# Kernel tuning notes

Measured on AMD Instinct MI355X. Metric: run time of the kernel, lower is better.

The kernel has to match this reference:

```python
import jax, jax.numpy as jnp
import numpy as np

B, S, H, F, E, K = 4, 2048, 1024, 3584, 8, 2
CAP_FACTOR = 1.25


def setup_inputs() -> dict:
    key = jax.random.key(0)
    k1, k2, k3, k4, k5 = jax.random.split(key, 5)
    s_h = 1.0 / np.sqrt(H)
    s_f = 1.0 / np.sqrt(F)
    return {
        "hidden_states": jax.random.normal(k1, (B, S, H), dtype=jnp.float32),
        "gate_w": jax.random.normal(k2, (E, H), dtype=jnp.float32) * s_h,
        "w1": jax.random.normal(k3, (E, H, F), dtype=jnp.float32) * s_h,
        "w2": jax.random.normal(k4, (E, F, H), dtype=jnp.float32) * s_f,
        "w3": jax.random.normal(k5, (E, H, F), dtype=jnp.float32) * s_h,
    }


def _moe_forward(hidden_states, gate_w, w1, w2, w3):
    b, s, h = hidden_states.shape
    dtype = hidden_states.dtype
    x = hidden_states.reshape(-1, h)  # [B*S, H]
    router_logits = x @ gate_w.T  # [B*S, E]
    expert_weights = jax.nn.softmax(router_logits.astype(jnp.float32), axis=1)
    _, selected_experts = jax.lax.top_k(expert_weights, K)  # [B*S, K]

    top_k_idx = selected_experts.reshape(b, s, K)
    probs = expert_weights.reshape(b, s, E)

    capacity = int(s * K / E * CAP_FACTOR)  # expert capacity per batch

    # dispatch/combine masks (Mixtral 'dropping' implementation)
    expert_mask = jax.nn.one_hot(top_k_idx, E, dtype=jnp.int32)  # [b,s,K,E]
    mask_fused = expert_mask.reshape(b, s * K, E)
    count_fused = jnp.cumsum(mask_fused, axis=1)  # running count per expert
    count = count_fused.reshape(b, s, K, E)
    trunc_mask = expert_mask * (count <= capacity).astype(jnp.int32)
    combined_mask = trunc_mask.sum(axis=2)  # [b,s,E]
    masked_probs = probs * combined_mask  # drop over-capacity tokens

    pos_fused = mask_fused * count_fused
    pos = pos_fused.reshape(b, s, K, E)
    combined_pos = pos.sum(axis=2) * combined_mask  # [b,s,E], 1-based slot
    pos_in_cap = jax.nn.one_hot(combined_pos, capacity + 1, dtype=jnp.int32)
    combine_mask = masked_probs[..., None] * pos_in_cap  # [b,s,E,cap+1]
    combine_mask = combine_mask[..., 1:].astype(dtype)  # drop slot 0 (dropped tokens)
    dispatch_mask = (combine_mask != 0).astype(dtype)  # [b,s,E,cap]

    # dispatch tokens into per-expert capacity buffers
    dispatch = jnp.einsum('bsm,bsec->ebcm', hidden_states, dispatch_mask)
    # expert FFN (SwiGLU)
    h1 = jnp.einsum('ebcm,emh->ebch', dispatch, w1)
    h3 = jnp.einsum('ebcm,emh->ebch', dispatch, w3)
    expert_out = jnp.einsum('ebch,ehm->ebcm', jax.nn.silu(h1) * h3, w2)
    # combine back to token order with routing probabilities
    final = jnp.einsum('ebcm,bsec->bsm', expert_out, combine_mask)
    return final


def reference(hidden_states, gate_w, w1, w2, w3):
    return _moe_forward(hidden_states, gate_w, w1, w2, w3)
```

## Files before the change

kernel.cpp:

```cpp
#include <hip/hip_runtime.h>
#include <hip/hip_bf16.h>
#include <math.h>

#define B_   4
#define S_   2048
#define H_   1024
#define F_   3584
#define E_   8
#define TOPK 2
#define CAP  640
#define M_   (B_*CAP)
#define NTOK (B_*S_)

typedef __attribute__((ext_vector_type(8))) short short8;
typedef __attribute__((ext_vector_type(4))) float f32x4;
typedef __attribute__((ext_vector_type(4))) unsigned short us4;

static __device__ __forceinline__ unsigned short f2bf(float f) {
  __hip_bfloat16 h = __float2bfloat16(f);
  return *reinterpret_cast<unsigned short*>(&h);
}
static __device__ __forceinline__ float bf2f(unsigned short u) {
  unsigned int x = ((unsigned int)u) << 16;
  float f;
  __builtin_memcpy(&f, &x, 4);
  return f;
}

static __device__ __forceinline__ void gload16(const void* g, void* l) {
  __builtin_amdgcn_global_load_lds((const __attribute__((address_space(1))) void*)g,
                                   (__attribute__((address_space(3))) void*)l, 16, 0, 0);
}

#define BAR() __builtin_amdgcn_s_barrier()
#define WLG() asm volatile("s_waitcnt lgkmcnt(0)" ::: "memory")
#define VM2() asm volatile("s_waitcnt vmcnt(2)" ::: "memory")
#define VM0() asm volatile("s_waitcnt vmcnt(0)" ::: "memory")

__global__ __launch_bounds__(64) void k_router(const float* __restrict__ hs,
                                               const float* __restrict__ gw,
                                               int* __restrict__ e01,
                                               float* __restrict__ p01,
                                               unsigned short* __restrict__ hsb) {
  int t = blockIdx.x;
  int lane = threadIdx.x;
  const float4* xv = (const float4*)(hs + (size_t)t * H_);
  float4 xr[4];
#pragma unroll
  for (int i = 0; i < 4; ++i) xr[i] = xv[lane + i * 64];
#pragma unroll
  for (int i = 0; i < 4; ++i) {
    us4 v = {f2bf(xr[i].x), f2bf(xr[i].y), f2bf(xr[i].z), f2bf(xr[i].w)};
    *(us4*)&hsb[(size_t)t * H_ + (size_t)(lane + i * 64) * 4] = v;
  }
  float logit[E_];
#pragma unroll
  for (int e = 0; e < E_; ++e) {
    const float4* gv = (const float4*)(gw + (size_t)e * H_);
    float acc = 0.f;
#pragma unroll
    for (int i = 0; i < 4; ++i) {
      float4 g = gv[lane + i * 64];
      acc += xr[i].x * g.x + xr[i].y * g.y + xr[i].z * g.z + xr[i].w * g.w;
    }
#pragma unroll
    for (int off = 32; off > 0; off >>= 1) acc += __shfl_xor(acc, off);
    logit[e] = acc;
  }
  float mx = logit[0];
#pragma unroll
  for (int e = 1; e < E_; ++e) mx = fmaxf(mx, logit[e]);
  float p[E_], s = 0.f;
#pragma unroll
  for (int e = 0; e < E_; ++e) { p[e] = expf(logit[e] - mx); s += p[e]; }
  float inv = 1.f / s;
  int e0 = 0;
#pragma unroll
  for (int e = 1; e < E_; ++e) if (p[e] > p[e0]) e0 = e;
  int e1 = (e0 == 0) ? 1 : 0;
#pragma unroll
  for (int e = 0; e < E_; ++e) if (e != e0 && p[e] > p[e1]) e1 = e;
  if (lane == 0) {
    e01[t * 2 + 0] = e0;
    e01[t * 2 + 1] = e1;
    p01[t * 2 + 0] = p[e0] * inv;
    p01[t * 2 + 1] = p[e1] * inv;
  }
}

__global__ __launch_bounds__(256) void k_positions(const int* __restrict__ e01,
                                                   int* __restrict__ pos,
                                                   int* __restrict__ disp) {
  int b = blockIdx.x, tid = threadIdx.x;
  __shared__ unsigned char eid[S_ * TOPK];
  __shared__ int part[256];
  for (int i = tid; i < E_ * CAP; i += 256)
    disp[((size_t)(i / CAP) * B_ + b) * CAP + (i % CAP)] = -1;
  for (int i = tid; i < S_ * TOPK; i += 256)
    eid[i] = (unsigned char)e01[b * S_ * TOPK + i];
  __syncthreads();
  const int per = (S_ * TOPK) / 256;
  int base = tid * per;
  for (int e = 0; e < E_; ++e) {
    int cnt = 0;
    for (int j = 0; j < per; ++j) cnt += (eid[base + j] == e) ? 1 : 0;
    part[tid] = cnt;
    __syncthreads();
    for (int off = 1; off < 256; off <<= 1) {
      int v = part[tid];
      int add = (tid >= off) ? part[tid - off] : 0;
      __syncthreads();
      part[tid] = v + add;
      __syncthreads();
    }
    int run = part[tid] - cnt;
    for (int j = 0; j < per; ++j) {
      int sl = base + j;
      if (eid[sl] == e) {
        ++run;
        int p = (run <= CAP) ? (run - 1) : -1;
        pos[b * S_ * TOPK + sl] = p;
        if (p >= 0) disp[((size_t)e * B_ + b) * CAP + p] = sl >> 1;
      }
    }
    __syncthreads();
  }
}

__global__ __launch_bounds__(256) void k_transpose(const float* __restrict__ in,
                                                   unsigned short* __restrict__ outp,
                                                   int R, int C, int ileave, int half,
                                                   size_t ostride_e) {
  __shared__ unsigned short ls[64][72];
  int e = blockIdx.z, tc = blockIdx.x, tr = blockIdx.y, tid = threadIdx.x;
  const float* src = in + (size_t)e * R * C + (size_t)tr * 64 * C + (size_t)tc * 64;
#pragma unroll
  for (int i = 0; i < 16; ++i) {
    int row = i * 4 + (tid >> 6), col = tid & 63;
    ls[row][col] = f2bf(src[(size_t)row * C + col]);
  }
  __syncthreads();
  unsigned short* dbase = outp + (size_t)e * ostride_e;
#pragma unroll
  for (int i = 0; i < 4; ++i) {
    int orow = i * 16 + (tid >> 4), oc = (tid & 15) * 4;
    int gr = tc * 64 + orow;
    int ri = ileave ? ((gr & ~15) * 2 + (gr & 15) + half * 16) : gr;
    us4 v = {ls[oc + 0][orow], ls[oc + 1][orow], ls[oc + 2][orow], ls[oc + 3][orow]};
    *(us4*)&dbase[(size_t)ri * R + tr * 64 + oc] = v;
  }
}

#define STAGE_A(d, h, t) {                                                    \
    gload16(pA0 + (size_t)(t) * 64 + (h) * 32, &lds[((d) * 2 + (h)) * 8192 + tid * 8]); \
  }
#define STAGE_B(d, h, t) {                                                    \
    gload16(srcB + (size_t)(t) * 64 + (h) * 32, &lds[32768 + ((d) * 2 + (h)) * 8192 + tid * 8]); \
  }
#define RD_A4(d, h) {                                                         \
    const unsigned short* _pa = &lds[((d) * 2 + (h)) * 8192 + aoff];          \
    _Pragma("unroll") for (int m = 0; m < 4; ++m)                             \
      a[m] = *(const short8*)&_pa[m * 512];                                   \
  }
#define RD_B4(d, h) {                                                         \
    const unsigned short* _pb = &lds[32768 + ((d) * 2 + (h)) * 8192 + boff];  \
    _Pragma("unroll") for (int n = 0; n < 4; ++n)                             \
      b[n] = *(const short8*)&_pb[n * 512];                                   \
  }
#define MFMA16() {                                                            \
    __builtin_amdgcn_s_setprio(1);                                            \
    _Pragma("unroll") for (int m = 0; m < 4; ++m)                             \
      _Pragma("unroll") for (int n = 0; n < 4; ++n)                           \
        acc[m][n] = __builtin_amdgcn_mfma_f32_16x16x32_bf16(a[m], b[n], acc[m][n], 0, 0, 0); \
    __builtin_amdgcn_s_setprio(0);                                            \
  }
#define BODY(P, tn) {                                                         \
    RD_A4(P, 0); RD_B4(P, 0); STAGE_A((P) ^ 1, 0, tn); STAGE_B((P) ^ 1, 0, tn); \
    WLG(); MFMA16(); VM2(); BAR();                                            \
    RD_A4(P, 1); RD_B4(P, 1); STAGE_A((P) ^ 1, 1, tn); STAGE_B((P) ^ 1, 1, tn); \
    WLG(); MFMA16(); VM2(); BAR();                                            \
  }
#define PEEL(P) {                                                             \
    RD_A4(P, 0); RD_B4(P, 0);                                                 \
    WLG(); MFMA16(); VM0(); BAR();                                            \
    RD_A4(P, 1); RD_B4(P, 1);                                                 \
    WLG(); MFMA16();                                                          \
  }

template <int KTOT, bool SWIGLU, bool GATHER, int MT, int NTN, int NTOTB, int SPLITK>
__global__ __launch_bounds__(1024, 4) void k_gemm256(const unsigned short* __restrict__ Aall,
                                                     const unsigned short* __restrict__ Ball,
                                                     unsigned short* __restrict__ Cout,
                                                     const int* __restrict__ disp) {
  constexpr int KSUB = KTOT / SPLITK;
  constexpr int NT = KSUB / 64;
  __shared__ __align__(16) unsigned short lds[65536];

  const int nwg = MT * NTN * E_ * SPLITK;
  int lid = blockIdx.x;
  int sw = (lid & 7) * (nwg >> 3) + (lid >> 3);
  constexpr int PER = MT * NTN;
  int ks = sw / (PER * E_);
  int rem2 = sw - ks * (PER * E_);
  int e = rem2 / PER;
  int rem = rem2 - e * PER;
  int tn = rem / MT, tm = rem - tn * MT;

  int tid = threadIdx.x, li = tid & 63, wid = tid >> 6;
  int wm = wid >> 2, wn = wid & 3;

  int rS = tid >> 2;
  int gS = (tid & 3) ^ ((tid >> 3) & 3);
  const unsigned short* pA0;
  if constexpr (GATHER) {
    int r0 = tm * 256 + rS;
    int b0 = r0 / CAP;
    int tok0 = disp[(size_t)e * B_ * CAP + r0];
    if (tok0 < 0) tok0 = 0;
    pA0 = Aall + ((size_t)b0 * S_ + tok0) * H_ + ks * KSUB + gS * 8;
  } else {
    pA0 = Aall + ((size_t)e * M_ + (size_t)tm * 256 + rS) * KTOT + ks * KSUB + gS * 8;
  }
  const unsigned short* srcB = Ball + ((size_t)e * NTOTB + (size_t)tn * 256 + rS) * KTOT + ks * KSUB + gS * 8;

  int sA = (li >> 4) ^ ((li >> 1) & 3);
  int aoff = (wm * 64 + (li & 15)) * 32 + sA * 8;
  int boff = (wn * 64 + (li & 15)) * 32 + sA * 8;

  f32x4 acc[4][4] = {};
  short8 a[4], b[4];

  STAGE_A(0, 0, 0); STAGE_B(0, 0, 0);
  STAGE_A(0, 1, 0); STAGE_B(0, 1, 0);
  VM2();
  BAR();

#pragma unroll 1
  for (int t = 0; t + 1 < NT - 1; t += 2) {
    BODY(0, t + 1);
    BODY(1, t + 2);
  }
  if constexpr (((NT - 1) & 1) != 0) {
    BODY(0, NT - 1);
  }
  if constexpr (((NT - 1) & 1) != 0) {
    PEEL(1);
  } else {
    PEEL(0);
  }

  int r0o = tm * 256 + wm * 64 + ((li >> 4) << 2);
  if constexpr (SWIGLU) {
    unsigned short* out = Cout + (size_t)e * M_ * F_;
#pragma unroll
    for (int m = 0; m < 4; ++m)
#pragma unroll
      for (int u = 0; u < 2; ++u) {
        int col = (tn * 8 + wn * 2 + u) * 16 + (li & 15);
#pragma unroll
        for (int j = 0; j < 4; ++j) {
          float h1 = acc[m][2 * u][j], h3 = acc[m][2 * u + 1][j];
          float sg = 1.f / (1.f + __expf(-h1));
          out[(size_t)(r0o + m * 16 + j) * F_ + col] = f2bf(h1 * sg * h3);
        }
      }
  } else {
    unsigned short* out = Cout + ((size_t)ks * E_ + e) * M_ * NTOTB;
#pragma unroll
    for (int m = 0; m < 4; ++m)
#pragma unroll
      for (int n = 0; n < 4; ++n) {
        int col = tn * 256 + wn * 64 + n * 16 + (li & 15);
#pragma unroll
        for (int j = 0; j < 4; ++j)
          out[(size_t)(r0o + m * 16 + j) * NTOTB + col] = f2bf(acc[m][n][j]);
      }
  }
}

__global__ __launch_bounds__(256) void k_combine(const unsigned short* __restrict__ Oe0,
                                                 const unsigned short* __restrict__ Oe1,
                                                 const int* __restrict__ e01,
                                                 const float* __restrict__ p01,
                                                 const int* __restrict__ pos,
                                                 float* __restrict__ outp) {
  int t = blockIdx.x;
  int b = t / S_;
  int tid = threadIdx.x;
  float4 acc = {0.f, 0.f, 0.f, 0.f};
#pragma unroll
  for (int k = 0; k < TOPK; ++k) {
    int p = pos[t * 2 + k];
    if (p >= 0) {
      int e = e01[t * 2 + k];
      float w = p01[t * 2 + k];
      size_t row = (size_t)e * M_ + (size_t)b * CAP + p;
      us4 v0 = *(const us4*)&Oe0[row * H_ + tid * 4];
      us4 v1 = *(const us4*)&Oe1[row * H_ + tid * 4];
      acc.x += w * (bf2f(v0[0]) + bf2f(v1[0]));
      acc.y += w * (bf2f(v0[1]) + bf2f(v1[1]));
      acc.z += w * (bf2f(v0[2]) + bf2f(v1[2]));
      acc.w += w * (bf2f(v0[3]) + bf2f(v1[3]));
    }
  }
  *(float4*)&outp[(size_t)t * H_ + tid * 4] = acc;
}

extern "C" void kernel_launch(void* const* d_in, const int* in_sizes, int n_in,
                              void* d_out, int out_size, void* d_ws, size_t ws_size,
                              hipStream_t stream) {
  const float* hs = (const float*)d_in[0];
  const float* gw = (const float*)d_in[1];
  const float* w1 = (const float*)d_in[2];
  const float* w2 = (const float*)d_in[3];
  const float* w3 = (const float*)d_in[4];

  char* ws = (char*)d_ws;
  size_t off = 0;
  auto take = [&](size_t bytes) -> char* {
    char* p = ws + off;
    off += (bytes + 255) & ~(size_t)255;
    return p;
  };
  int*            e01  = (int*)take((size_t)NTOK * 2 * 4);
  float*          p01  = (float*)take((size_t)NTOK * 2 * 4);
  int*            pos  = (int*)take((size_t)NTOK * 2 * 4);
  int*            disp = (int*)take((size_t)E_ * B_ * CAP * 4);
  unsigned short* w13t = (unsigned short*)take((size_t)E_ * 2 * F_ * H_ * 2);
  unsigned short* w2t  = (unsigned short*)take((size_t)E_ * H_ * F_ * 2);
  unsigned short* hsb  = (unsigned short*)take((size_t)NTOK * H_ * 2);
  unsigned short* act  = (unsigned short*)take((size_t)E_ * M_ * F_ * 2);
  unsigned short* oe   = (unsigned short*)take((size_t)2 * E_ * M_ * H_ * 2);

  k_router<<<NTOK, 64, 0, stream>>>(hs, gw, e01, p01, hsb);
  k_positions<<<B_, 256, 0, stream>>>(e01, pos, disp);
  k_transpose<<<dim3(F_ / 64, H_ / 64, E_), 256, 0, stream>>>(w1, w13t, H_, F_, 1, 0, (size_t)2 * F_ * H_);
  k_transpose<<<dim3(F_ / 64, H_ / 64, E_), 256, 0, stream>>>(w3, w13t, H_, F_, 1, 1, (size_t)2 * F_ * H_);
  k_transpose<<<dim3(H_ / 64, F_ / 64, E_), 256, 0, stream>>>(w2, w2t, F_, H_, 0, 0, (size_t)H_ * F_);
  k_gemm256<H_, true, true, M_ / 256, (2 * F_) / 256, 2 * F_, 1>
      <<<(M_ / 256) * ((2 * F_) / 256) * E_, 1024, 0, stream>>>(hsb, w13t, act, disp);
  k_gemm256<F_, false, false, M_ / 256, H_ / 256, H_, 2>
      <<<(M_ / 256) * (H_ / 256) * E_ * 2, 1024, 0, stream>>>(act, w2t, oe, disp);
  k_combine<<<NTOK, 256, 0, stream>>>(oe, oe + (size_t)E_ * M_ * H_, e01, p01, pos, (float*)d_out);
}
```

Baseline: 599.2 us.

## Split GEMM kernels and give down-projection 512-thread blocks with 128x64 warp tiles

The shared templated GEMM becomes two kernels. The gate/up kernel keeps its 1024-thread, 64x64-per-warp layout. The down-projection kernel now runs 512 threads per block, and each warp covers a 128x64 output tile with 8x4 accumulators. Each thread issues two global-to-LDS loads per stage, and the pipeline is split into four MFMA phases with vmcnt(4) waits. The aim is more operand reuse per LDS read and per wave, at the cost of a doubled accumulator register footprint and lower occupancy.

New measurement: 614.0 us. +2.5%, slower.

```diff
diff --git a/kernel.cpp b/kernel.cpp
--- a/kernel.cpp
+++ b/kernel.cpp
@@ -34,6 +34,7 @@
 
 #define BAR() __builtin_amdgcn_s_barrier()
 #define WLG() asm volatile("s_waitcnt lgkmcnt(0)" ::: "memory")
+#define VM4() asm volatile("s_waitcnt vmcnt(4)" ::: "memory")
 #define VM2() asm volatile("s_waitcnt vmcnt(2)" ::: "memory")
 #define VM0() asm volatile("s_waitcnt vmcnt(0)" ::: "memory")
 
@@ -151,47 +152,164 @@
   }
 }
 
-#define STAGE_A(d, h, t) {                                                    \
+#define STAGE_A10(d, h, t) {                                                  \
     gload16(pA0 + (size_t)(t) * 64 + (h) * 32, &lds[((d) * 2 + (h)) * 8192 + tid * 8]); \
   }
-#define STAGE_B(d, h, t) {                                                    \
+#define STAGE_B10(d, h, t) {                                                  \
     gload16(srcB + (size_t)(t) * 64 + (h) * 32, &lds[32768 + ((d) * 2 + (h)) * 8192 + tid * 8]); \
   }
-#define RD_A4(d, h) {                                                         \
+#define RD_A10(d, h) {                                                        \
     const unsigned short* _pa = &lds[((d) * 2 + (h)) * 8192 + aoff];          \
     _Pragma("unroll") for (int m = 0; m < 4; ++m)                             \
       a[m] = *(const short8*)&_pa[m * 512];                                   \
   }
-#define RD_B4(d, h) {                                                         \
+#define RD_B10(d, h) {                                                        \
     const unsigned short* _pb = &lds[32768 + ((d) * 2 + (h)) * 8192 + boff];  \
     _Pragma("unroll") for (int n = 0; n < 4; ++n)                             \
       b[n] = *(const short8*)&_pb[n * 512];                                   \
   }
-#define MFMA16() {                                                            \
+#define MFMA10() {                                                            \
     __builtin_amdgcn_s_setprio(1);                                            \
     _Pragma("unroll") for (int m = 0; m < 4; ++m)                             \
       _Pragma("unroll") for (int n = 0; n < 4; ++n)                           \
         acc[m][n] = __builtin_amdgcn_mfma_f32_16x16x32_bf16(a[m], b[n], acc[m][n], 0, 0, 0); \
     __builtin_amdgcn_s_setprio(0);                                            \
   }
-#define BODY(P, tn) {                                                         \
-    RD_A4(P, 0); RD_B4(P, 0); STAGE_A((P) ^ 1, 0, tn); STAGE_B((P) ^ 1, 0, tn); \
-    WLG(); MFMA16(); VM2(); BAR();                                            \
-    RD_A4(P, 1); RD_B4(P, 1); STAGE_A((P) ^ 1, 1, tn); STAGE_B((P) ^ 1, 1, tn); \
-    WLG(); MFMA16(); VM2(); BAR();                                            \
-  }
-#define PEEL(P) {                                                             \
-    RD_A4(P, 0); RD_B4(P, 0);                                                 \
-    WLG(); MFMA16(); VM0(); BAR();                                            \
-    RD_A4(P, 1); RD_B4(P, 1);                                                 \
-    WLG(); MFMA16();                                                          \
-  }
-
-template <int KTOT, bool SWIGLU, bool GATHER, int MT, int NTN, int NTOTB, int SPLITK>
-__global__ __launch_bounds__(1024, 4) void k_gemm256(const unsigned short* __restrict__ Aall,
-                                                     const unsigned short* __restrict__ Ball,
-                                                     unsigned short* __restrict__ Cout,
-                                                     const int* __restrict__ disp) {
+#define BODY10(P, tn) {                                                       \
+    RD_A10(P, 0); RD_B10(P, 0); STAGE_A10((P) ^ 1, 0, tn); STAGE_B10((P) ^ 1, 0, tn); \
+    WLG(); MFMA10(); VM2(); BAR();                                            \
+    RD_A10(P, 1); RD_B10(P, 1); STAGE_A10((P) ^ 1, 1, tn); STAGE_B10((P) ^ 1, 1, tn); \
+    WLG(); MFMA10(); VM2(); BAR();                                            \
+  }
+#define PEEL10(P) {                                                           \
+    RD_A10(P, 0); RD_B10(P, 0);                                               \
+    WLG(); MFMA10(); VM0(); BAR();                                            \
+    RD_A10(P, 1); RD_B10(P, 1);                                               \
+    WLG(); MFMA10();                                                          \
+  }
+
+template <int KTOT, int MT, int NTN, int NTOTB>
+__global__ __launch_bounds__(1024, 4) void k_gemm1(const unsigned short* __restrict__ Aall,
+                                                   const unsigned short* __restrict__ Ball,
+                                                   unsigned short* __restrict__ Cout,
+                                                   const int* __restrict__ disp) {
+  constexpr int NT = KTOT / 64;
+  __shared__ __align__(16) unsigned short lds[65536];
+
+  const int nwg = MT * NTN * E_;
+  int lid = blockIdx.x;
+  int sw = (lid & 7) * (nwg >> 3) + (lid >> 3);
+  constexpr int PER = MT * NTN;
+  int e = sw / PER;
+  int rem = sw - e * PER;
+  int tn = rem / MT, tm = rem - tn * MT;
+
+  int tid = threadIdx.x, li = tid & 63, wid = tid >> 6;
+  int wm = wid >> 2, wn = wid & 3;
+
+  int rS = tid >> 2;
+  int gS = (tid & 3) ^ ((tid >> 3) & 3);
+  int r0 = tm * 256 + rS;
+  int b0 = r0 / CAP;
+  int tok0 = disp[(size_t)e * B_ * CAP + r0];
+  if (tok0 < 0) tok0 = 0;
+  const unsigned short* pA0 = Aall + ((size_t)b0 * S_ + tok0) * H_ + gS * 8;
+  const unsigned short* srcB = Ball + ((size_t)e * NTOTB + (size_t)tn * 256 + rS) * KTOT + gS * 8;
+
+  int sA = (li >> 4) ^ ((li >> 1) & 3);
+  int aoff = (wm * 64 + (li & 15)) * 32 + sA * 8;
+  int boff = (wn * 64 + (li & 15)) * 32 + sA * 8;
+
+  f32x4 acc[4][4] = {};
+  short8 a[4], b[4];
+
+  STAGE_A10(0, 0, 0); STAGE_B10(0, 0, 0);
+  STAGE_A10(0, 1, 0); STAGE_B10(0, 1, 0);
+  VM2();
+  BAR();
+
+#pragma unroll 1
+  for (int t = 0; t + 1 < NT - 1; t += 2) {
+    BODY10(0, t + 1);
+    BODY10(1, t + 2);
+  }
+  if constexpr (((NT - 1) & 1) != 0) {
+    BODY10(0, NT - 1);
+  }
+  if constexpr (((NT - 1) & 1) != 0) {
+    PEEL10(1);
+  } else {
+    PEEL10(0);
+  }
+
+  int r0o = tm * 256 + wm * 64 + ((li >> 4) << 2);
+  unsigned short* out = Cout + (size_t)e * M_ * F_;
+#pragma unroll
+  for (int m = 0; m < 4; ++m)
+#pragma unroll
+    for (int u = 0; u < 2; ++u) {
+      int col = (tn * 8 + wn * 2 + u) * 16 + (li & 15);
+#pragma unroll
+      for (int j = 0; j < 4; ++j) {
+        float h1 = acc[m][2 * u][j], h3 = acc[m][2 * u + 1][j];
+        float sg = 1.f / (1.f + __expf(-h1));
+        out[(size_t)(r0o + m * 16 + j) * F_ + col] = f2bf(h1 * sg * h3);
+      }
+    }
+}
+
+#define STAGE_A5(d, h, t) {                                                   \
+    size_t _o = (size_t)(t) * 64 + (h) * 32;                                  \
+    gload16(pA0 + _o, &lds[((d) * 2 + (h)) * 8192 + tid * 8]);                \
+    gload16(pA1 + _o, &lds[((d) * 2 + (h)) * 8192 + tid * 8 + 4096]);         \
+  }
+#define STAGE_B5(d, h, t) {                                                   \
+    size_t _o = (size_t)(t) * 64 + (h) * 32;                                  \
+    gload16(srcB + _o, &lds[32768 + ((d) * 2 + (h)) * 8192 + tid * 8]);       \
+    gload16(srcB + (size_t)128 * KTOT + _o, &lds[32768 + ((d) * 2 + (h)) * 8192 + tid * 8 + 4096]); \
+  }
+#define RD_A5(d, h, mh) {                                                     \
+    const unsigned short* _pa = &lds[((d) * 2 + (h)) * 8192 + aoff + (mh) * 2048]; \
+    _Pragma("unroll") for (int j = 0; j < 4; ++j)                             \
+      a[j] = *(const short8*)&_pa[j * 512];                                   \
+  }
+#define RD_B5(d, h) {                                                         \
+    const unsigned short* _pb = &lds[32768 + ((d) * 2 + (h)) * 8192 + boff];  \
+    _Pragma("unroll") for (int n = 0; n < 4; ++n)                             \
+      b[n] = *(const short8*)&_pb[n * 512];                                   \
+  }
+#define MFMA5(mh) {                                                           \
+    __builtin_amdgcn_s_setprio(1);                                            \
+    _Pragma("unroll") for (int j = 0; j < 4; ++j)                             \
+      _Pragma("unroll") for (int n = 0; n < 4; ++n)                           \
+        acc[(mh) * 4 + j][n] = __builtin_amdgcn_mfma_f32_16x16x32_bf16(a[j], b[n], acc[(mh) * 4 + j][n], 0, 0, 0); \
+    __builtin_amdgcn_s_setprio(0);                                            \
+  }
+#define BODY5(P, tn) {                                                        \
+    RD_A5(P, 0, 0); RD_B5(P, 0); STAGE_A5((P) ^ 1, 0, tn);                    \
+    WLG(); MFMA5(0); BAR();                                                   \
+    RD_A5(P, 0, 1); STAGE_B5((P) ^ 1, 0, tn);                                 \
+    WLG(); MFMA5(1); VM4(); BAR();                                            \
+    RD_A5(P, 1, 0); RD_B5(P, 1); STAGE_A5((P) ^ 1, 1, tn);                    \
+    WLG(); MFMA5(0); BAR();                                                   \
+    RD_A5(P, 1, 1); STAGE_B5((P) ^ 1, 1, tn);                                 \
+    WLG(); MFMA5(1); VM4(); BAR();                                            \
+  }
+#define PEEL5(P) {                                                            \
+    RD_A5(P, 0, 0); RD_B5(P, 0);                                              \
+    WLG(); MFMA5(0); BAR();                                                   \
+    RD_A5(P, 0, 1);                                                           \
+    WLG(); MFMA5(1); VM0(); BAR();                                            \
+    RD_A5(P, 1, 0); RD_B5(P, 1);                                              \
+    WLG(); MFMA5(0); BAR();                                                   \
+    RD_A5(P, 1, 1);                                                           \
+    WLG(); MFMA5(1);                                                          \
+  }
+
+template <int KTOT, int MT, int NTN, int NTOTB, int SPLITK>
+__global__ __launch_bounds__(512, 2) void k_gemm2(const unsigned short* __restrict__ Aall,
+                                                  const unsigned short* __restrict__ Ball,
+                                                  unsigned short* __restrict__ Cout) {
   constexpr int KSUB = KTOT / SPLITK;
   constexpr int NT = KSUB / 64;
   __shared__ __align__(16) unsigned short lds[65536];
@@ -211,71 +329,47 @@
 
   int rS = tid >> 2;
   int gS = (tid & 3) ^ ((tid >> 3) & 3);
-  const unsigned short* pA0;
-  if constexpr (GATHER) {
-    int r0 = tm * 256 + rS;
-    int b0 = r0 / CAP;
-    int tok0 = disp[(size_t)e * B_ * CAP + r0];
-    if (tok0 < 0) tok0 = 0;
-    pA0 = Aall + ((size_t)b0 * S_ + tok0) * H_ + ks * KSUB + gS * 8;
-  } else {
-    pA0 = Aall + ((size_t)e * M_ + (size_t)tm * 256 + rS) * KTOT + ks * KSUB + gS * 8;
-  }
+  const unsigned short* pA0 = Aall + ((size_t)e * M_ + (size_t)tm * 256 + rS) * KTOT + ks * KSUB + gS * 8;
+  const unsigned short* pA1 = pA0 + (size_t)128 * KTOT;
   const unsigned short* srcB = Ball + ((size_t)e * NTOTB + (size_t)tn * 256 + rS) * KTOT + ks * KSUB + gS * 8;
 
   int sA = (li >> 4) ^ ((li >> 1) & 3);
-  int aoff = (wm * 64 + (li & 15)) * 32 + sA * 8;
+  int aoff = (wm * 128 + (li & 15)) * 32 + sA * 8;
   int boff = (wn * 64 + (li & 15)) * 32 + sA * 8;
 
-  f32x4 acc[4][4] = {};
+  f32x4 acc[8][4] = {};
   short8 a[4], b[4];
 
-  STAGE_A(0, 0, 0); STAGE_B(0, 0, 0);
-  STAGE_A(0, 1, 0); STAGE_B(0, 1, 0);
-  VM2();
+  STAGE_A5(0, 0, 0); STAGE_B5(0, 0, 0);
+  STAGE_A5(0, 1, 0); STAGE_B5(0, 1, 0);
+  VM4();
   BAR();
 
 #pragma unroll 1
   for (int t = 0; t + 1 < NT - 1; t += 2) {
-    BODY(0, t + 1);
-    BODY(1, t + 2);
+    BODY5(0, t + 1);
+    BODY5(1, t + 2);
   }
   if constexpr (((NT - 1) & 1) != 0) {
-    BODY(0, NT - 1);
+    BODY5(0, NT - 1);
   }
   if constexpr (((NT - 1) & 1) != 0) {
-    PEEL(1);
+    PEEL5(1);
   } else {
-    PEEL(0);
-  }
-
-  int r0o = tm * 256 + wm * 64 + ((li >> 4) << 2);
-  if constexpr (SWIGLU) {
-    unsigned short* out = Cout + (size_t)e * M_ * F_;
-#pragma unroll
-    for (int m = 0; m < 4; ++m)
-#pragma unroll
-      for (int u = 0; u < 2; ++u) {
-        int col = (tn * 8 + wn * 2 + u) * 16 + (li & 15);
-#pragma unroll
-        for (int j = 0; j < 4; ++j) {
-          float h1 = acc[m][2 * u][j], h3 = acc[m][2 * u + 1][j];
-          float sg = 1.f / (1.f + __expf(-h1));
-          out[(size_t)(r0o + m * 16 + j) * F_ + col] = f2bf(h1 * sg * h3);
-        }
-      }
-  } else {
-    unsigned short* out = Cout + ((size_t)ks * E_ + e) * M_ * NTOTB;
-#pragma unroll
-    for (int m = 0; m < 4; ++m)
-#pragma unroll
-      for (int n = 0; n < 4; ++n) {
-        int col = tn * 256 + wn * 64 + n * 16 + (li & 15);
-#pragma unroll
-        for (int j = 0; j < 4; ++j)
-          out[(size_t)(r0o + m * 16 + j) * NTOTB + col] = f2bf(acc[m][n][j]);
-      }
-  }
+    PEEL5(0);
+  }
+
+  int r0o = tm * 256 + wm * 128 + ((li >> 4) << 2);
+  unsigned short* out = Cout + ((size_t)ks * E_ + e) * M_ * NTOTB;
+#pragma unroll
+  for (int m = 0; m < 8; ++m)
+#pragma unroll
+    for (int n = 0; n < 4; ++n) {
+      int col = tn * 256 + wn * 64 + n * 16 + (li & 15);
+#pragma unroll
+      for (int j = 0; j < 4; ++j)
+        out[(size_t)(r0o + m * 16 + j) * NTOTB + col] = f2bf(acc[m][n][j]);
+    }
 }
 
 __global__ __launch_bounds__(256) void k_combine(const unsigned short* __restrict__ Oe0,
@@ -337,9 +431,9 @@
   k_transpose<<<dim3(F_ / 64, H_ / 64, E_), 256, 0, stream>>>(w1, w13t, H_, F_, 1, 0, (size_t)2 * F_ * H_);
   k_transpose<<<dim3(F_ / 64, H_ / 64, E_), 256, 0, stream>>>(w3, w13t, H_, F_, 1, 1, (size_t)2 * F_ * H_);
   k_transpose<<<dim3(H_ / 64, F_ / 64, E_), 256, 0, stream>>>(w2, w2t, F_, H_, 0, 0, (size_t)H_ * F_);
-  k_gemm256<H_, true, true, M_ / 256, (2 * F_) / 256, 2 * F_, 1>
+  k_gemm1<H_, M_ / 256, (2 * F_) / 256, 2 * F_>
       <<<(M_ / 256) * ((2 * F_) / 256) * E_, 1024, 0, stream>>>(hsb, w13t, act, disp);
-  k_gemm256<F_, false, false, M_ / 256, H_ / 256, H_, 2>
-      <<<(M_ / 256) * (H_ / 256) * E_ * 2, 1024, 0, stream>>>(act, w2t, oe, disp);
+  k_gemm2<F_, M_ / 256, H_ / 256, H_, 2>
+      <<<(M_ / 256) * (H_ / 256) * E_ * 2, 512, 0, stream>>>(act, w2t, oe);
   k_combine<<<NTOK, 256, 0, stream>>>(oe, oe + (size_t)E_ * M_ * H_, e01, p01, pos, (float*)d_out);
 }
```
